# Kernel optimization log

Measured on AMD Instinct MI355X. Metric: run time of the kernel, lower is better.

Reference implementation:

```python
import math
import jax, jax.numpy as jnp
import numpy as np

T = 32
BETA_START, BETA_END = 1e-4, 1e-2
ACTION_DIM, ACTION_HORIZON = 4, 16
CHUNK = ACTION_DIM * ACTION_HORIZON  # 64
COND_DIM = 256
TIME_EMB_DIM = 32
HIDDEN = 256
IN_DIM = CHUNK + TIME_EMB_DIM + COND_DIM  # 352
B = 65536


def setup_inputs() -> dict:
    key = jax.random.key(0)
    ks = jax.random.split(key, 12)
    def lin(k, fan_in, fan_out):
        bound = 1.0 / math.sqrt(fan_in)
        kw, kb = jax.random.split(k)
        W = jax.random.uniform(kw, (fan_in, fan_out), jnp.float32, -bound, bound)
        b = jax.random.uniform(kb, (fan_out,), jnp.float32, -bound, bound)
        return W, b
    W1, b1 = lin(ks[0], IN_DIM, HIDDEN)
    W2, b2 = lin(ks[1], HIDDEN, HIDDEN)
    W3, b3 = lin(ks[2], HIDDEN, HIDDEN)
    W4, b4 = lin(ks[3], HIDDEN, CHUNK)
    cond = jax.random.normal(ks[4], (B, COND_DIM), jnp.float32)
    x_init = jax.random.normal(ks[5], (B, CHUNK), jnp.float32)
    return {"cond": cond, "x_init": x_init,
            "W1": W1, "b1": b1, "W2": W2, "b2": b2,
            "W3": W3, "b3": b3, "W4": W4, "b4": b4}


def reference(cond, x_init, W1, b1, W2, b2, W3, b3, W4, b4):
    betas = jnp.linspace(BETA_START, BETA_END, T).astype(jnp.float32)
    alphas = 1.0 - betas
    alpha_bar = jnp.cumprod(alphas)
    # sinusoidal time-embedding frequencies
    freqs = jnp.exp(jnp.linspace(0.0, math.log(1000.0), TIME_EMB_DIM // 2)).astype(jnp.float32)

    t_steps = jnp.arange(T - 1, -1, -1)            # T-1 ... 0
    noise_keys = jax.random.split(jax.random.key(42), T)

    def denoise(x_t, t_step):
        args = t_step.astype(jnp.float32) * freqs          # [16]
        t_emb = jnp.concatenate([jnp.sin(args), jnp.cos(args)])  # [32]
        t_emb_b = jnp.broadcast_to(t_emb, (x_t.shape[0], TIME_EMB_DIM))
        x = jnp.concatenate([x_t, t_emb_b, cond], axis=-1)  # [B, 352]
        h = jax.nn.silu(x @ W1 + b1)
        h = jax.nn.silu(h @ W2 + b2)
        h = jax.nn.silu(h @ W3 + b3)
        return h @ W4 + b4                                  # [B, 64]

    def step(x_t, inp):
        t_step, nkey = inp
        eps = denoise(x_t, t_step)
        abar_t = alpha_bar[t_step]
        x0_pred = (x_t - jnp.sqrt(1.0 - abar_t) * eps) / jnp.sqrt(abar_t)
        noise = jax.random.normal(nkey, x_t.shape, jnp.float32)
        x_next = jnp.where(
            t_step > 0,
            jnp.sqrt(alphas[t_step]) * x0_pred + jnp.sqrt(betas[t_step]) * noise,
            x0_pred,
        )
        return x_next, None

    x_final, _ = jax.lax.scan(step, x_init, (t_steps, noise_keys))
    return x_final.reshape(-1, ACTION_HORIZON, ACTION_DIM)
```

## Files before the change

kernel.cpp:

```cpp
#include <hip/hip_runtime.h>
#include <stdint.h>
#include <stddef.h>

#define NROWS 65536
#define BM 256
#define NBLK (NROWS / BM)

typedef __attribute__((ext_vector_type(8))) short bf16x8;
typedef __attribute__((ext_vector_type(16))) float f32x16;

struct Consts {
  unsigned k0[32]; unsigned k1[32];
  float s1d[32];
  float sqa[32];
  float sqb[32];
  float inva[32];
};

__device__ __forceinline__ unsigned short f2bf(float f) {
  unsigned u = __float_as_uint(f);
  u += 0x7fffu + ((u >> 16) & 1u);
  return (unsigned short)(u >> 16);
}

__device__ __forceinline__ unsigned cvtpk(float lo, float hi) {
  unsigned r;
  asm("v_cvt_pk_bf16_f32 %0, %1, %2" : "=v"(r) : "v"(lo), "v"(hi));
  return r;
}

__device__ __forceinline__ float silu(float v) {
  return v * __builtin_amdgcn_rcpf(1.0f + __expf(-v));
}

__device__ __forceinline__ void gload_lds16(const void* g, void* l) {
  __builtin_amdgcn_global_load_lds(
      (const __attribute__((address_space(1))) unsigned int*)g,
      (__attribute__((address_space(3))) unsigned int*)l, 16, 0, 0);
}

__device__ __forceinline__ float noise_normal(unsigned k0, unsigned k1, unsigned idx) {
  unsigned x0 = 0u, x1 = idx;
  unsigned ks2 = k0 ^ k1 ^ 0x1BD11BDAu;
  x0 += k0; x1 += k1;
#define TFR(r) { x0 += x1; x1 = (x1 << r) | (x1 >> (32 - r)); x1 ^= x0; }
  TFR(13) TFR(15) TFR(26) TFR(6)
  x0 += k1;  x1 += ks2 + 1u;
  TFR(17) TFR(29) TFR(16) TFR(24)
  x0 += ks2; x1 += k0 + 2u;
  TFR(13) TFR(15) TFR(26) TFR(6)
  x0 += k0;  x1 += k1 + 3u;
  TFR(17) TFR(29) TFR(16) TFR(24)
  x0 += k1;  x1 += ks2 + 4u;
  TFR(13) TFR(15) TFR(26) TFR(6)
  x0 += ks2; x1 += k0 + 5u;
#undef TFR
  unsigned bits = x0 ^ x1;
  float f = __uint_as_float((bits >> 9) | 0x3f800000u) - 1.0f;
  const float mn = -0.99999994f;
  float u = f * 2.0f + mn;
  u = fmaxf(mn, u);
  float w = -__logf(fmaf(-u, u, 1.0f));
  float p;
  if (w < 5.0f) {
    w -= 2.5f;
    p = 2.81022636e-08f;
    p = fmaf(p, w, 3.43273939e-07f);
    p = fmaf(p, w, -3.5233877e-06f);
    p = fmaf(p, w, -4.39150654e-06f);
    p = fmaf(p, w, 0.00021858087f);
    p = fmaf(p, w, -0.00125372503f);
    p = fmaf(p, w, -0.00417768164f);
    p = fmaf(p, w, 0.246640727f);
    p = fmaf(p, w, 1.50140941f);
  } else {
    w = sqrtf(w) - 3.0f;
    p = -0.000200214257f;
    p = fmaf(p, w, 0.000100950558f);
    p = fmaf(p, w, 0.00134934322f);
    p = fmaf(p, w, -0.00367342844f);
    p = fmaf(p, w, 0.00573950773f);
    p = fmaf(p, w, -0.0076224613f);
    p = fmaf(p, w, 0.00943887047f);
    p = fmaf(p, w, 1.00167406f);
    p = fmaf(p, w, 2.83297682f);
  }
  return 1.41421356f * (p * u);
}

__global__ void pack_w_k(const float* __restrict__ W1, const float* __restrict__ W2,
                         const float* __restrict__ W3, const float* __restrict__ W4,
                         unsigned short* __restrict__ wbuf) {
  int o = blockIdx.x * 256 + threadIdx.x;
  int f = o >> 9, q = o & 511, l = q >> 3, e = q & 7;
  int l31 = l & 31, kex = (l >> 5) * 8 + e;
  float v;
  if (f < 32) {
    int p = f >> 3, ctl = (f >> 2) & 1, kt = f & 3;
    v = W1[(16 * kt + kex) * 256 + 32 * (2 * p + ctl) + l31];
  } else if (f < 160) {
    int g = f - 32; int cp = g >> 5, ctl = (g >> 4) & 1, kt = g & 15;
    v = W2[(16 * kt + kex) * 256 + 32 * (2 * cp + ctl) + l31];
  } else if (f < 288) {
    int g = f - 160; int cp = g >> 5, ctl = (g >> 4) & 1, kt = g & 15;
    v = W3[(16 * kt + kex) * 256 + 32 * (2 * cp + ctl) + l31];
  } else if (f < 320) {
    int g = f - 288; int ctl = g >> 4, kt = g & 15;
    v = W4[(16 * kt + kex) * 64 + 32 * ctl + l31];
  } else {
    int g = f - 320; int cp = g >> 5, ctl = (g >> 4) & 1, kt = g & 15;
    v = W1[(96 + 16 * kt + kex) * 256 + 32 * (2 * cp + ctl) + l31];
  }
  wbuf[o] = f2bf(v);
}

__global__ void b1eff_k(const float* __restrict__ W1, const float* __restrict__ b1,
                        float* __restrict__ b1eff) {
  int t = blockIdx.x, n = threadIdx.x;
  float acc = b1[n];
#pragma unroll
  for (int j = 0; j < 16; ++j) {
    float arg = (float)t * expf((float)j * (6.907755278982137f / 15.0f));
    acc += sinf(arg) * W1[(64 + j) * 256 + n] + cosf(arg) * W1[(80 + j) * 256 + n];
  }
  int sw = ((n >> 5) << 5) + (((n >> 2) & 1) << 4) + (n & 3) + (((n >> 3) & 3) << 2);
  b1eff[t * 256 + sw] = acc;
}

#define MF32(W, B, C) __builtin_amdgcn_mfma_f32_32x32x16_bf16((W), (B), (C), 0, 0, 0)

__global__ __launch_bounds__(256) void pcond_k(const float* __restrict__ cond,
                                               const unsigned short* __restrict__ wbuf,
                                               unsigned short* __restrict__ P) {
  const int tid = threadIdx.x;
  const int wave = tid >> 6, lane = tid & 63;
  const int l31 = lane & 31, kh = lane >> 5;
  const int row = blockIdx.x * 128 + wave * 32 + l31;

  bf16x8 cf[16];
#pragma unroll
  for (int kt = 0; kt < 16; ++kt) {
    const float* p = cond + (size_t)row * 256 + 16 * kt + 8 * kh;
    float4 a = *(const float4*)p;
    float4 b = *(const float4*)(p + 4);
    union { bf16x8 f; unsigned u[4]; } cu;
    cu.u[0] = cvtpk(a.x, a.y); cu.u[1] = cvtpk(a.z, a.w);
    cu.u[2] = cvtpk(b.x, b.y); cu.u[3] = cvtpk(b.z, b.w);
    cf[kt] = cu.f;
  }

#define PSTORE(AV, CT) do { \
  uint4 u0_, u1_; \
  u0_.x = cvtpk(AV[0], AV[1]);   u0_.y = cvtpk(AV[2], AV[3]); \
  u0_.z = cvtpk(AV[4], AV[5]);   u0_.w = cvtpk(AV[6], AV[7]); \
  u1_.x = cvtpk(AV[8], AV[9]);   u1_.y = cvtpk(AV[10], AV[11]); \
  u1_.z = cvtpk(AV[12], AV[13]); u1_.w = cvtpk(AV[14], AV[15]); \
  uint4* pp_ = (uint4*)(P + ((size_t)((CT) * 2 + kh) * 65536 + (size_t)row) * 16); \
  pp_[0] = u0_; pp_[1] = u1_; \
} while (0)

#pragma unroll
  for (int cp = 0; cp < 4; ++cp) {
    f32x16 a0, a1;
#pragma unroll
    for (int z = 0; z < 16; ++z) { a0[z] = 0.0f; a1[z] = 0.0f; }
#pragma unroll
    for (int kt = 0; kt < 16; ++kt) {
      bf16x8 w0 = *(const bf16x8*)(wbuf + (size_t)(320 + cp * 32 + kt) * 512 + lane * 8);
      bf16x8 w1 = *(const bf16x8*)(wbuf + (size_t)(320 + cp * 32 + 16 + kt) * 512 + lane * 8);
      a0 = MF32(w0, cf[kt], a0);
      a1 = MF32(w1, cf[kt], a1);
    }
    PSTORE(a0, 2 * cp);
    PSTORE(a1, 2 * cp + 1);
  }
#undef PSTORE
}

__device__ __forceinline__ void issue_chunk(const unsigned short* __restrict__ wsW,
                                            const float* __restrict__ b1eff,
                                            unsigned short* smem, int k, int tid) {
  if (k >= 320) return;
  int c = k % 10;
  unsigned short* dst = smem + (k & 1) * 16384;
  const unsigned short* src = wsW + c * 16384;
#pragma unroll
  for (int i = 0; i < 4; ++i) {
    int off = (i * 512 + tid) * 8;
    gload_lds16(src + off, dst + off);
  }
  if (c == 9 && tid < 64) {
    int tn = 30 - k / 10;
    if (tn >= 0) gload_lds16(b1eff + tn * 256 + tid * 4, (float*)(smem + 65536) + tid * 4);
  }
}

#define FRAGBUILD(vv, D0, D1) do { \
  unsigned c0_ = cvtpk(vv[0], vv[1]),  c2_ = cvtpk(vv[2], vv[3]); \
  unsigned c1_ = cvtpk(vv[4], vv[5]),  c3_ = cvtpk(vv[6], vv[7]); \
  asm volatile("v_permlane32_swap_b32 %0, %1" : "+v"(c0_), "+v"(c1_)); \
  asm volatile("v_permlane32_swap_b32 %0, %1" : "+v"(c2_), "+v"(c3_)); \
  union { bf16x8 f; unsigned u[4]; } F0_; \
  F0_.u[0] = c0_; F0_.u[1] = c2_; F0_.u[2] = c1_; F0_.u[3] = c3_; (D0) = F0_.f; \
  unsigned d0_ = cvtpk(vv[8], vv[9]),   d2_ = cvtpk(vv[10], vv[11]); \
  unsigned d1_ = cvtpk(vv[12], vv[13]), d3_ = cvtpk(vv[14], vv[15]); \
  asm volatile("v_permlane32_swap_b32 %0, %1" : "+v"(d0_), "+v"(d1_)); \
  asm volatile("v_permlane32_swap_b32 %0, %1" : "+v"(d2_), "+v"(d3_)); \
  union { bf16x8 f; unsigned u[4]; } F1_; \
  F1_.u[0] = d0_; F1_.u[1] = d2_; F1_.u[2] = d1_; F1_.u[3] = d3_; (D1) = F1_.f; \
} while (0)

#define ACTF(AV, BOFF, CT, D0, D1) do { \
  const float* bp_ = biasF + (BOFF) + (CT) * 32 + kh * 16; \
  float4 b0_ = *(const float4*)bp_; \
  float4 b1_ = *(const float4*)(bp_ + 4); \
  float4 b2_ = *(const float4*)(bp_ + 8); \
  float4 b3_ = *(const float4*)(bp_ + 12); \
  float vv[16]; \
  vv[0]=AV[0]+b0_.x; vv[1]=AV[1]+b0_.y; vv[2]=AV[2]+b0_.z; vv[3]=AV[3]+b0_.w; \
  vv[4]=AV[4]+b1_.x; vv[5]=AV[5]+b1_.y; vv[6]=AV[6]+b1_.z; vv[7]=AV[7]+b1_.w; \
  vv[8]=AV[8]+b2_.x; vv[9]=AV[9]+b2_.y; vv[10]=AV[10]+b2_.z; vv[11]=AV[11]+b2_.w; \
  vv[12]=AV[12]+b3_.x; vv[13]=AV[13]+b3_.y; vv[14]=AV[14]+b3_.z; vv[15]=AV[15]+b3_.w; \
  _Pragma("unroll") for (int r_ = 0; r_ < 16; ++r_) vv[r_] = silu(vv[r_]); \
  FRAGBUILD(vv, D0, D1); \
} while (0)

#define ACTF0(AV, D0, D1) do { \
  float vv[16]; \
  _Pragma("unroll") for (int r_ = 0; r_ < 16; ++r_) vv[r_] = silu(AV[r_]); \
  FRAGBUILD(vv, D0, D1); \
} while (0)

#define PDEC(ACC, PA, PB, CT) do { \
  const float* bb_ = biasF + (CT) * 32 + kh * 16; \
  float4 b0_ = *(const float4*)bb_; \
  float4 b1_ = *(const float4*)(bb_ + 4); \
  float4 b2_ = *(const float4*)(bb_ + 8); \
  float4 b3_ = *(const float4*)(bb_ + 12); \
  float ba_[16] = {b0_.x,b0_.y,b0_.z,b0_.w, b1_.x,b1_.y,b1_.z,b1_.w, \
                   b2_.x,b2_.y,b2_.z,b2_.w, b3_.x,b3_.y,b3_.z,b3_.w}; \
  unsigned uu_[8] = {PA.x, PA.y, PA.z, PA.w, PB.x, PB.y, PB.z, PB.w}; \
  _Pragma("unroll") for (int w_ = 0; w_ < 8; ++w_) { \
    ACC[2 * w_]     = __uint_as_float(uu_[w_] << 16)          + ba_[2 * w_]; \
    ACC[2 * w_ + 1] = __uint_as_float(uu_[w_] & 0xffff0000u)  + ba_[2 * w_ + 1]; } \
} while (0)

#define NEXTCHUNK() do { __syncthreads(); ++ck; \
  bufp = smem + (ck & 1) * 16384; \
  issue_chunk(wsW, b1eff, smem, ck + 1, tid); } while (0)

#define ZER16(A) { _Pragma("unroll") for (int z_ = 0; z_ < 16; ++z_) (A)[z_] = 0.0f; }

#define ZQUAD(CI) if (t > 0) { \
  _Pragma("unroll") for (int q_ = 4 * (CI); q_ <= 4 * (CI) + 3; ++q_) { \
    int n_ = 32 * (q_ >> 4) + 8 * ((q_ >> 2) & 3) + 4 * kh + (q_ & 3); \
    z[q_] = noise_normal(kk0, kk1, (unsigned)(row * 64 + n_)); } }

__global__ __launch_bounds__(512, 1) void diff_main(
    const float* __restrict__ x_init,
    const float* __restrict__ b2g, const float* __restrict__ b3g, const float* __restrict__ b4g,
    const unsigned short* __restrict__ wsW, const float* __restrict__ b1eff,
    const unsigned short* __restrict__ Pglob,
    float* __restrict__ out, Consts C) {
  extern __shared__ unsigned short smem[];
  float* xlds  = (float*)(smem + 32768);
  float* biasF = (float*)(smem + 65536);

  const int tid = threadIdx.x;
  const int wave = tid >> 6, lane = tid & 63;
  const int l31 = lane & 31, kh = lane >> 5;
  const int lane8 = lane * 8;
  const int row = blockIdx.x * BM + wave * 32 + l31;

  for (int i = tid; i < 576; i += 512) {
    float v; int n, base;
    if (i < 256)      { v = b2g[i];       n = i;       base = 256; }
    else if (i < 512) { v = b3g[i - 256]; n = i - 256; base = 512; }
    else              { v = b4g[i - 512]; n = i - 512; base = 768; }
    int sw = ((n >> 5) << 5) + (((n >> 2) & 1) << 4) + (n & 3) + (((n >> 3) & 3) << 2);
    biasF[base + sw] = v;
  }
  if (tid < 64) gload_lds16(b1eff + 31 * 256 + tid * 4, biasF + tid * 4);

#pragma unroll
  for (int ct4 = 0; ct4 < 2; ++ct4) {
#pragma unroll
    for (int g = 0; g < 4; ++g) {
      float4 xv = *(const float4*)(x_init + (size_t)row * 64 + 32 * ct4 + 8 * g + 4 * kh);
      *(float4*)(xlds + wave * 2048 + (ct4 * 4 + g) * 256 + lane * 4) = xv;
    }
  }

  int ck = 0;
  const unsigned short* bufp = smem;
  issue_chunk(wsW, b1eff, smem, 0, tid);
  __syncthreads();
  issue_chunk(wsW, b1eff, smem, 1, tid);

  bf16x8 hhA[16], hhB[16];
  float z[32];

#pragma unroll 1
  for (int t = 31; t >= 0; --t) {
    unsigned kk0 = C.k0[31 - t], kk1 = C.k1[31 - t];

    {
      bf16x8 xf[4];
      {
        float vv[16];
#pragma unroll
        for (int ct4 = 0; ct4 < 2; ++ct4) {
#pragma unroll
          for (int g = 0; g < 4; ++g) {
            float4 xv = *(const float4*)(xlds + wave * 2048 + (ct4 * 4 + g) * 256 + lane * 4);
            vv[4 * g + 0] = xv.x; vv[4 * g + 1] = xv.y; vv[4 * g + 2] = xv.z; vv[4 * g + 3] = xv.w;
          }
          if (ct4 == 0) { FRAGBUILD(vv, xf[0], xf[1]); } else { FRAGBUILD(vv, xf[2], xf[3]); }
        }
      }
#pragma unroll
      for (int p = 0; p < 4; ++p) {
        const uint4* Pa = (const uint4*)(Pglob + ((size_t)(4 * p + kh) * 65536 + (size_t)row) * 16);
        const uint4* Pb = (const uint4*)(Pglob + ((size_t)(4 * p + 2 + kh) * 65536 + (size_t)row) * 16);
        uint4 pa0 = Pa[0], pa1 = Pa[1];
        uint4 pb0 = Pb[0], pb1 = Pb[1];
        f32x16 a0, a1;
        PDEC(a0, pa0, pa1, 2 * p);
        PDEC(a1, pb0, pb1, 2 * p + 1);
        __builtin_amdgcn_s_setprio(1);
#pragma unroll
        for (int kt = 0; kt < 4; ++kt) {
          bf16x8 w0 = *(const bf16x8*)(bufp + (p * 8 + kt) * 512 + lane8);
          bf16x8 w1 = *(const bf16x8*)(bufp + (p * 8 + 4 + kt) * 512 + lane8);
          a0 = MF32(w0, xf[kt], a0);
          a1 = MF32(w1, xf[kt], a1);
        }
        __builtin_amdgcn_s_setprio(0);
        ACTF0(a0, hhA[4 * p],     hhA[4 * p + 1]);
        ACTF0(a1, hhA[4 * p + 2], hhA[4 * p + 3]);
      }
    }
    NEXTCHUNK();

#pragma unroll
    for (int p = 0; p < 4; ++p) {
      f32x16 a0, a1; ZER16(a0); ZER16(a1);
      __builtin_amdgcn_s_setprio(1);
#pragma unroll
      for (int kt = 0; kt < 16; ++kt) {
        bf16x8 w0 = *(const bf16x8*)(bufp + kt * 512 + lane8);
        bf16x8 w1 = *(const bf16x8*)(bufp + (16 + kt) * 512 + lane8);
        a0 = MF32(w0, hhA[kt], a0);
        a1 = MF32(w1, hhA[kt], a1);
      }
      __builtin_amdgcn_s_setprio(0);
      ACTF(a0, 256, 2 * p,     hhB[4 * p],     hhB[4 * p + 1]);
      ACTF(a1, 256, 2 * p + 1, hhB[4 * p + 2], hhB[4 * p + 3]);
      ZQUAD(p);
      NEXTCHUNK();
    }

#pragma unroll
    for (int p = 0; p < 4; ++p) {
      f32x16 a0, a1; ZER16(a0); ZER16(a1);
      __builtin_amdgcn_s_setprio(1);
#pragma unroll
      for (int kt = 0; kt < 16; ++kt) {
        bf16x8 w0 = *(const bf16x8*)(bufp + kt * 512 + lane8);
        bf16x8 w1 = *(const bf16x8*)(bufp + (16 + kt) * 512 + lane8);
        a0 = MF32(w0, hhB[kt], a0);
        a1 = MF32(w1, hhB[kt], a1);
      }
      __builtin_amdgcn_s_setprio(0);
      ACTF(a0, 512, 2 * p,     hhA[4 * p],     hhA[4 * p + 1]);
      ACTF(a1, 512, 2 * p + 1, hhA[4 * p + 2], hhA[4 * p + 3]);
      ZQUAD(4 + p);
      NEXTCHUNK();
    }

    {
      f32x16 e0, e1; ZER16(e0); ZER16(e1);
      __builtin_amdgcn_s_setprio(1);
#pragma unroll
      for (int kt = 0; kt < 16; ++kt) {
        bf16x8 w0 = *(const bf16x8*)(bufp + kt * 512 + lane8);
        bf16x8 w1 = *(const bf16x8*)(bufp + (16 + kt) * 512 + lane8);
        e0 = MF32(w0, hhA[kt], e0);
        e1 = MF32(w1, hhA[kt], e1);
      }
      __builtin_amdgcn_s_setprio(0);

      float s1d = C.s1d[t], sqa = C.sqa[t], sqb = C.sqb[t], inva = C.inva[t];
#pragma unroll
      for (int ct4 = 0; ct4 < 2; ++ct4) {
        const float* bp4 = biasF + 768 + ct4 * 32 + kh * 16;
#pragma unroll
        for (int g = 0; g < 4; ++g) {
          float4 bb = *(const float4*)(bp4 + 4 * g);
          float* xq = xlds + wave * 2048 + (ct4 * 4 + g) * 256 + lane * 4;
          float4 xv = *(const float4*)xq;
          float xa[4] = {xv.x, xv.y, xv.z, xv.w};
          float ba[4] = {bb.x, bb.y, bb.z, bb.w};
#pragma unroll
          for (int j = 0; j < 4; ++j) {
            int r = 4 * g + j;
            float eps = (ct4 ? e1[r] : e0[r]) + ba[j];
            float x0p = fmaf(-s1d, eps, xa[j]) * inva;
            if (t > 0) {
              xa[j] = fmaf(sqa, x0p, sqb * z[ct4 * 16 + 4 * g + j]);
            } else {
              xa[j] = x0p;
            }
          }
          if (t > 0) {
            float4 xs; xs.x = xa[0]; xs.y = xa[1]; xs.z = xa[2]; xs.w = xa[3];
            *(float4*)xq = xs;
          } else {
            float4 ov; ov.x = xa[0]; ov.y = xa[1]; ov.z = xa[2]; ov.w = xa[3];
            *(float4*)(out + (size_t)row * 64 + 32 * ct4 + 8 * g + 4 * kh) = ov;
          }
        }
      }
      NEXTCHUNK();
    }
  }
}

static void host_threefry(unsigned k0, unsigned k1, unsigned x0, unsigned x1,
                          unsigned* o0, unsigned* o1) {
  unsigned ks2 = k0 ^ k1 ^ 0x1BD11BDAu;
  x0 += k0; x1 += k1;
#define HR(r) { x0 += x1; x1 = (x1 << r) | (x1 >> (32 - r)); x1 ^= x0; }
  HR(13) HR(15) HR(26) HR(6)
  x0 += k1;  x1 += ks2 + 1u;
  HR(17) HR(29) HR(16) HR(24)
  x0 += ks2; x1 += k0 + 2u;
  HR(13) HR(15) HR(26) HR(6)
  x0 += k0;  x1 += k1 + 3u;
  HR(17) HR(29) HR(16) HR(24)
  x0 += k1;  x1 += ks2 + 4u;
  HR(13) HR(15) HR(26) HR(6)
  x0 += ks2; x1 += k0 + 5u;
#undef HR
  *o0 = x0; *o1 = x1;
}

extern "C" void kernel_launch(void* const* d_in, const int* in_sizes, int n_in,
                              void* d_out, int out_size, void* d_ws, size_t ws_size,
                              hipStream_t stream) {
  const float* cond   = (const float*)d_in[0];
  const float* x_init = (const float*)d_in[1];
  const float* W1 = (const float*)d_in[2];
  const float* b1 = (const float*)d_in[3];
  const float* W2 = (const float*)d_in[4];
  const float* b2 = (const float*)d_in[5];
  const float* W3 = (const float*)d_in[6];
  const float* b3 = (const float*)d_in[7];
  const float* W4 = (const float*)d_in[8];
  const float* b4 = (const float*)d_in[9];

  unsigned short* wbuf = (unsigned short*)d_ws;
  float* b1eff = (float*)((char*)d_ws + 491520);
  unsigned short* Pbuf = (unsigned short*)((char*)d_ws + 524288);

  pack_w_k<<<960, 256, 0, stream>>>(W1, W2, W3, W4, wbuf);
  b1eff_k<<<32, 256, 0, stream>>>(W1, b1, b1eff);
  pcond_k<<<512, 256, 0, stream>>>(cond, wbuf, Pbuf);

  Consts C;
  for (int i = 0; i < 32; ++i) {
    unsigned o0, o1;
    host_threefry(0u, 42u, 0u, (unsigned)i, &o0, &o1);
    C.k0[i] = o0; C.k1[i] = o1;
  }
  {
    const float bstep = (0.01f - 0.0001f) / 31.0f;
    float abar = 1.0f;
    for (int t = 0; t < 32; ++t) {
      float beta_t = 0.0001f + bstep * (float)t;
      float alpha_t = 1.0f - beta_t;
      abar *= (1.0f - (0.0001f + bstep * (float)t));
      C.s1d[t]  = sqrtf(1.0f - abar);
      C.sqa[t]  = sqrtf(alpha_t);
      C.sqb[t]  = sqrtf(beta_t);
      C.inva[t] = 1.0f / sqrtf(abar);
    }
  }

  const int shmem = 134400;
  hipFuncSetAttribute((const void*)diff_main, hipFuncAttributeMaxDynamicSharedMemorySize, 160 * 1024);
  diff_main<<<NBLK, 512, shmem, stream>>>(x_init, b2, b3, b4,
                                          wbuf, b1eff, Pbuf, (float*)d_out, C);
}
```

Measured before the change: 1.582 ms.

## Halve block size and weight chunks to fit two blocks per CU

Result: slower. 1.803 ms (+14.0%).

```diff
diff --git a/kernel.cpp b/kernel.cpp
--- a/kernel.cpp
+++ b/kernel.cpp
@@ -3,7 +3,7 @@
 #include <stddef.h>
 
 #define NROWS 65536
-#define BM 256
+#define BM 128
 #define NBLK (NROWS / BM)
 
 typedef __attribute__((ext_vector_type(8))) short bf16x8;
@@ -96,16 +96,16 @@
   int l31 = l & 31, kex = (l >> 5) * 8 + e;
   float v;
   if (f < 32) {
-    int p = f >> 3, ctl = (f >> 2) & 1, kt = f & 3;
+    int p = f >> 3, r = f & 7, kt = r >> 1, ctl = r & 1;
     v = W1[(16 * kt + kex) * 256 + 32 * (2 * p + ctl) + l31];
   } else if (f < 160) {
-    int g = f - 32; int cp = g >> 5, ctl = (g >> 4) & 1, kt = g & 15;
+    int g = f - 32; int cp = g >> 5, r = g & 31, kt = r >> 1, ctl = r & 1;
     v = W2[(16 * kt + kex) * 256 + 32 * (2 * cp + ctl) + l31];
   } else if (f < 288) {
-    int g = f - 160; int cp = g >> 5, ctl = (g >> 4) & 1, kt = g & 15;
+    int g = f - 160; int cp = g >> 5, r = g & 31, kt = r >> 1, ctl = r & 1;
     v = W3[(16 * kt + kex) * 256 + 32 * (2 * cp + ctl) + l31];
   } else if (f < 320) {
-    int g = f - 288; int ctl = g >> 4, kt = g & 15;
+    int g = f - 288; int kt = g >> 1, ctl = g & 1;
     v = W4[(16 * kt + kex) * 64 + 32 * ctl + l31];
   } else {
     int g = f - 320; int cp = g >> 5, ctl = (g >> 4) & 1, kt = g & 15;
@@ -180,18 +180,18 @@
 __device__ __forceinline__ void issue_chunk(const unsigned short* __restrict__ wsW,
                                             const float* __restrict__ b1eff,
                                             unsigned short* smem, int k, int tid) {
-  if (k >= 320) return;
-  int c = k % 10;
-  unsigned short* dst = smem + (k & 1) * 16384;
-  const unsigned short* src = wsW + c * 16384;
+  if (k >= 640) return;
+  int c = k % 20;
+  unsigned short* dst = smem + (k & 1) * 8192;
+  const unsigned short* src = wsW + c * 8192;
 #pragma unroll
   for (int i = 0; i < 4; ++i) {
-    int off = (i * 512 + tid) * 8;
+    int off = (i * 256 + tid) * 8;
     gload_lds16(src + off, dst + off);
   }
-  if (c == 9 && tid < 64) {
-    int tn = 30 - k / 10;
-    if (tn >= 0) gload_lds16(b1eff + tn * 256 + tid * 4, (float*)(smem + 65536) + tid * 4);
+  if (c == 19 && tid < 64) {
+    int tn = 30 - k / 20;
+    if (tn >= 0) gload_lds16(b1eff + tn * 256 + tid * 4, (float*)(smem + 32768) + tid * 4);
   }
 }
 
@@ -246,25 +246,20 @@
 } while (0)
 
 #define NEXTCHUNK() do { __syncthreads(); ++ck; \
-  bufp = smem + (ck & 1) * 16384; \
+  bufp = smem + (ck & 1) * 8192; \
   issue_chunk(wsW, b1eff, smem, ck + 1, tid); } while (0)
 
 #define ZER16(A) { _Pragma("unroll") for (int z_ = 0; z_ < 16; ++z_) (A)[z_] = 0.0f; }
 
-#define ZQUAD(CI) if (t > 0) { \
-  _Pragma("unroll") for (int q_ = 4 * (CI); q_ <= 4 * (CI) + 3; ++q_) { \
-    int n_ = 32 * (q_ >> 4) + 8 * ((q_ >> 2) & 3) + 4 * kh + (q_ & 3); \
-    z[q_] = noise_normal(kk0, kk1, (unsigned)(row * 64 + n_)); } }
-
-__global__ __launch_bounds__(512, 1) void diff_main(
+__global__ __launch_bounds__(256, 1) void diff_main(
     const float* __restrict__ x_init,
     const float* __restrict__ b2g, const float* __restrict__ b3g, const float* __restrict__ b4g,
     const unsigned short* __restrict__ wsW, const float* __restrict__ b1eff,
     const unsigned short* __restrict__ Pglob,
     float* __restrict__ out, Consts C) {
   extern __shared__ unsigned short smem[];
-  float* xlds  = (float*)(smem + 32768);
-  float* biasF = (float*)(smem + 65536);
+  float* xlds  = (float*)(smem + 16384);
+  float* biasF = (float*)(smem + 32768);
 
   const int tid = threadIdx.x;
   const int wave = tid >> 6, lane = tid & 63;
@@ -272,7 +267,7 @@
   const int lane8 = lane * 8;
   const int row = blockIdx.x * BM + wave * 32 + l31;
 
-  for (int i = tid; i < 576; i += 512) {
+  for (int i = tid; i < 576; i += 256) {
     float v; int n, base;
     if (i < 256)      { v = b2g[i];       n = i;       base = 256; }
     else if (i < 512) { v = b3g[i - 256]; n = i - 256; base = 512; }
@@ -298,13 +293,11 @@
   issue_chunk(wsW, b1eff, smem, 1, tid);
 
   bf16x8 hhA[16], hhB[16];
-  float z[32];
 
 #pragma unroll 1
   for (int t = 31; t >= 0; --t) {
-    unsigned kk0 = C.k0[31 - t], kk1 = C.k1[31 - t];
-
-    {
+#pragma unroll
+    for (int half = 0; half < 2; ++half) {
       bf16x8 xf[4];
       {
         float vv[16];
@@ -319,7 +312,8 @@
         }
       }
 #pragma unroll
-      for (int p = 0; p < 4; ++p) {
+      for (int pp = 0; pp < 2; ++pp) {
+        int p = half * 2 + pp;
         const uint4* Pa = (const uint4*)(Pglob + ((size_t)(4 * p + kh) * 65536 + (size_t)row) * 16);
         const uint4* Pb = (const uint4*)(Pglob + ((size_t)(4 * p + 2 + kh) * 65536 + (size_t)row) * 16);
         uint4 pa0 = Pa[0], pa1 = Pa[1];
@@ -330,8 +324,8 @@
         __builtin_amdgcn_s_setprio(1);
 #pragma unroll
         for (int kt = 0; kt < 4; ++kt) {
-          bf16x8 w0 = *(const bf16x8*)(bufp + (p * 8 + kt) * 512 + lane8);
-          bf16x8 w1 = *(const bf16x8*)(bufp + (p * 8 + 4 + kt) * 512 + lane8);
+          bf16x8 w0 = *(const bf16x8*)(bufp + (pp * 8 + kt * 2 + 0) * 512 + lane8);
+          bf16x8 w1 = *(const bf16x8*)(bufp + (pp * 8 + kt * 2 + 1) * 512 + lane8);
           a0 = MF32(w0, xf[kt], a0);
           a1 = MF32(w1, xf[kt], a1);
         }
@@ -339,42 +333,60 @@
         ACTF0(a0, hhA[4 * p],     hhA[4 * p + 1]);
         ACTF0(a1, hhA[4 * p + 2], hhA[4 * p + 3]);
       }
-    }
-    NEXTCHUNK();
-
-#pragma unroll
-    for (int p = 0; p < 4; ++p) {
+      NEXTCHUNK();
+    }
+
+#pragma unroll
+    for (int cp = 0; cp < 4; ++cp) {
       f32x16 a0, a1; ZER16(a0); ZER16(a1);
       __builtin_amdgcn_s_setprio(1);
 #pragma unroll
-      for (int kt = 0; kt < 16; ++kt) {
-        bf16x8 w0 = *(const bf16x8*)(bufp + kt * 512 + lane8);
-        bf16x8 w1 = *(const bf16x8*)(bufp + (16 + kt) * 512 + lane8);
+      for (int kt = 0; kt < 8; ++kt) {
+        bf16x8 w0 = *(const bf16x8*)(bufp + (kt * 2 + 0) * 512 + lane8);
+        bf16x8 w1 = *(const bf16x8*)(bufp + (kt * 2 + 1) * 512 + lane8);
         a0 = MF32(w0, hhA[kt], a0);
         a1 = MF32(w1, hhA[kt], a1);
       }
       __builtin_amdgcn_s_setprio(0);
-      ACTF(a0, 256, 2 * p,     hhB[4 * p],     hhB[4 * p + 1]);
-      ACTF(a1, 256, 2 * p + 1, hhB[4 * p + 2], hhB[4 * p + 3]);
-      ZQUAD(p);
-      NEXTCHUNK();
-    }
-
-#pragma unroll
-    for (int p = 0; p < 4; ++p) {
+      NEXTCHUNK();
+      __builtin_amdgcn_s_setprio(1);
+#pragma unroll
+      for (int kt = 0; kt < 8; ++kt) {
+        bf16x8 w0 = *(const bf16x8*)(bufp + (kt * 2 + 0) * 512 + lane8);
+        bf16x8 w1 = *(const bf16x8*)(bufp + (kt * 2 + 1) * 512 + lane8);
+        a0 = MF32(w0, hhA[8 + kt], a0);
+        a1 = MF32(w1, hhA[8 + kt], a1);
+      }
+      __builtin_amdgcn_s_setprio(0);
+      ACTF(a0, 256, 2 * cp,     hhB[4 * cp],     hhB[4 * cp + 1]);
+      ACTF(a1, 256, 2 * cp + 1, hhB[4 * cp + 2], hhB[4 * cp + 3]);
+      NEXTCHUNK();
+    }
+
+#pragma unroll
+    for (int cp = 0; cp < 4; ++cp) {
       f32x16 a0, a1; ZER16(a0); ZER16(a1);
       __builtin_amdgcn_s_setprio(1);
 #pragma unroll
-      for (int kt = 0; kt < 16; ++kt) {
-        bf16x8 w0 = *(const bf16x8*)(bufp + kt * 512 + lane8);
-        bf16x8 w1 = *(const bf16x8*)(bufp + (16 + kt) * 512 + lane8);
+      for (int kt = 0; kt < 8; ++kt) {
+        bf16x8 w0 = *(const bf16x8*)(bufp + (kt * 2 + 0) * 512 + lane8);
+        bf16x8 w1 = *(const bf16x8*)(bufp + (kt * 2 + 1) * 512 + lane8);
         a0 = MF32(w0, hhB[kt], a0);
         a1 = MF32(w1, hhB[kt], a1);
       }
       __builtin_amdgcn_s_setprio(0);
-      ACTF(a0, 512, 2 * p,     hhA[4 * p],     hhA[4 * p + 1]);
-      ACTF(a1, 512, 2 * p + 1, hhA[4 * p + 2], hhA[4 * p + 3]);
-      ZQUAD(4 + p);
+      NEXTCHUNK();
+      __builtin_amdgcn_s_setprio(1);
+#pragma unroll
+      for (int kt = 0; kt < 8; ++kt) {
+        bf16x8 w0 = *(const bf16x8*)(bufp + (kt * 2 + 0) * 512 + lane8);
+        bf16x8 w1 = *(const bf16x8*)(bufp + (kt * 2 + 1) * 512 + lane8);
+        a0 = MF32(w0, hhB[8 + kt], a0);
+        a1 = MF32(w1, hhB[8 + kt], a1);
+      }
+      __builtin_amdgcn_s_setprio(0);
+      ACTF(a0, 512, 2 * cp,     hhA[4 * cp],     hhA[4 * cp + 1]);
+      ACTF(a1, 512, 2 * cp + 1, hhA[4 * cp + 2], hhA[4 * cp + 3]);
       NEXTCHUNK();
     }
 
@@ -382,15 +394,26 @@
       f32x16 e0, e1; ZER16(e0); ZER16(e1);
       __builtin_amdgcn_s_setprio(1);
 #pragma unroll
-      for (int kt = 0; kt < 16; ++kt) {
-        bf16x8 w0 = *(const bf16x8*)(bufp + kt * 512 + lane8);
-        bf16x8 w1 = *(const bf16x8*)(bufp + (16 + kt) * 512 + lane8);
+      for (int kt = 0; kt < 8; ++kt) {
+        bf16x8 w0 = *(const bf16x8*)(bufp + (kt * 2 + 0) * 512 + lane8);
+        bf16x8 w1 = *(const bf16x8*)(bufp + (kt * 2 + 1) * 512 + lane8);
         e0 = MF32(w0, hhA[kt], e0);
         e1 = MF32(w1, hhA[kt], e1);
       }
       __builtin_amdgcn_s_setprio(0);
+      NEXTCHUNK();
+      __builtin_amdgcn_s_setprio(1);
+#pragma unroll
+      for (int kt = 0; kt < 8; ++kt) {
+        bf16x8 w0 = *(const bf16x8*)(bufp + (kt * 2 + 0) * 512 + lane8);
+        bf16x8 w1 = *(const bf16x8*)(bufp + (kt * 2 + 1) * 512 + lane8);
+        e0 = MF32(w0, hhA[8 + kt], e0);
+        e1 = MF32(w1, hhA[8 + kt], e1);
+      }
+      __builtin_amdgcn_s_setprio(0);
 
       float s1d = C.s1d[t], sqa = C.sqa[t], sqb = C.sqb[t], inva = C.inva[t];
+      unsigned kk0 = C.k0[31 - t], kk1 = C.k1[31 - t];
 #pragma unroll
       for (int ct4 = 0; ct4 < 2; ++ct4) {
         const float* bp4 = biasF + 768 + ct4 * 32 + kh * 16;
@@ -407,7 +430,9 @@
             float eps = (ct4 ? e1[r] : e0[r]) + ba[j];
             float x0p = fmaf(-s1d, eps, xa[j]) * inva;
             if (t > 0) {
-              xa[j] = fmaf(sqa, x0p, sqb * z[ct4 * 16 + 4 * g + j]);
+              int n = 32 * ct4 + 8 * g + 4 * kh + j;
+              float z = noise_normal(kk0, kk1, (unsigned)(row * 64 + n));
+              xa[j] = fmaf(sqa, x0p, sqb * z);
             } else {
               xa[j] = x0p;
             }
@@ -487,8 +512,8 @@
     }
   }
 
-  const int shmem = 134400;
-  hipFuncSetAttribute((const void*)diff_main, hipFuncAttributeMaxDynamicSharedMemorySize, 160 * 1024);
-  diff_main<<<NBLK, 512, shmem, stream>>>(x_init, b2, b3, b4,
+  const int shmem = 68864;
+  hipFuncSetAttribute((const void*)diff_main, hipFuncAttributeMaxDynamicSharedMemorySize, 81920);
+  diff_main<<<NBLK, 256, shmem, stream>>>(x_init, b2, b3, b4,
                                           wbuf, b1eff, Pbuf, (float*)d_out, C);
 }
```
